# Kernel tuning notes

Measured on AMD Instinct MI355X. Metric: run time of the kernel, lower is better.

Reference implementation:

```python
import jax, jax.numpy as jnp
import numpy as np

ROPE_BASE = 10000.0

def apply_rope(x):
    # x: (BS, T, H, hd). 1D RoPE over temporal axis with rotate-half convention.
    BS, T, H, hd = x.shape
    half = hd // 2
    inv_freq = 1.0 / (ROPE_BASE ** (jnp.arange(0, half, dtype=jnp.float32) / half))
    angles = jnp.arange(T, dtype=jnp.float32)[:, None] * inv_freq[None, :]  # (T, half)
    cos = jnp.concatenate([jnp.cos(angles), jnp.cos(angles)], axis=-1)[None, :, None, :]  # (1,T,1,hd)
    sin = jnp.concatenate([jnp.sin(angles), jnp.sin(angles)], axis=-1)[None, :, None, :]
    x1, x2 = x[..., :half], x[..., half:]
    x_rot = jnp.concatenate([-x2, x1], axis=-1)
    return (x * cos + x_rot * sin).astype(x.dtype)

def setup_inputs() -> dict:
    key = jax.random.key(0)
    ks = jax.random.split(key, 7)
    B, T_p, T_f, S, d = 4, 8, 8, 256, 512
    v_p = jax.random.normal(ks[0], (B, T_p, S, d), dtype=jnp.float32)
    v_f = jax.random.normal(ks[1], (B, T_f, S, d), dtype=jnp.float32)
    a_p = jax.random.normal(ks[2], (B, T_p, d), dtype=jnp.float32)
    a_f = jax.random.normal(ks[3], (B, T_f, d), dtype=jnp.float32)
    W_qkv = jax.random.normal(ks[4], (d, 3 * d), dtype=jnp.float32) * (d ** -0.5)
    W_proj = jax.random.normal(ks[5], (d, d), dtype=jnp.float32) * (d ** -0.5)
    b_proj = jnp.zeros((d,), dtype=jnp.float32)
    return {"v_p": v_p, "v_f": v_f, "a_p": a_p, "a_f": a_f,
            "W_qkv": W_qkv, "W_proj": W_proj, "b_proj": b_proj}

def reference(v_p, v_f, a_p, a_f, W_qkv, W_proj, b_proj):
    num_heads = 8
    B, T_p, S, d = v_p.shape
    T_f = v_f.shape[1]
    hd = d // num_heads
    scale = hd ** -0.5

    # rearrange 'b t s d -> (b s) t d'
    vp = jnp.transpose(v_p, (0, 2, 1, 3)).reshape(B * S, T_p, d)
    vf = jnp.transpose(v_f, (0, 2, 1, 3)).reshape(B * S, T_f, d)
    # repeat 'b t d -> (b s) t d'
    ap = jnp.broadcast_to(a_p[:, None], (B, S, T_p, d)).reshape(B * S, T_p, d)
    af = jnp.broadcast_to(a_f[:, None], (B, S, T_f, d)).reshape(B * S, T_f, d)

    tokens = jnp.concatenate([vp, vf, ap, af], axis=1)  # (BS, total_T, d)
    BS, total_T = tokens.shape[0], tokens.shape[1]

    qkv = tokens @ W_qkv  # (BS, total_T, 3d), no bias
    q, k, v = jnp.split(qkv, 3, axis=-1)
    q = q.reshape(BS, total_T, num_heads, hd)
    k = k.reshape(BS, total_T, num_heads, hd)
    v = v.reshape(BS, total_T, num_heads, hd)

    q = apply_rope(q)
    k = apply_rope(k)

    # joint bidirectional attention over total_T
    attn = jnp.einsum('bthd,bThd->bhtT', q, k) * scale
    attn = jax.nn.softmax(attn, axis=-1)
    out = jnp.einsum('bhtT,bThd->bthd', attn, v).reshape(BS, total_T, d)

    out = out @ W_proj + b_proj

    vp_o = out[:, :T_p]
    vf_o = out[:, T_p:T_p + T_f]
    ap_o = out[:, T_p + T_f:T_p + T_f + T_p]
    af_o = out[:, T_p + T_f + T_p:]

    # '(b s) t d -> b t s d'
    vp_o = jnp.transpose(vp_o.reshape(B, S, T_p, d), (0, 2, 1, 3))
    vf_o = jnp.transpose(vf_o.reshape(B, S, T_f, d), (0, 2, 1, 3))
    # '(b s) t d -> b s t d' then mean over s
    ap_o = ap_o.reshape(B, S, T_p, d).mean(axis=1)
    af_o = af_o.reshape(B, S, T_f, d).mean(axis=1)
    return (vp_o, vf_o, ap_o, af_o)
```

## Files before the change

kernel.cpp:

```cpp
#include <hip/hip_runtime.h>
#include <math.h>

#define BB   4
#define SS   256
#define DD   512
#define HH   8
#define HD   64
#define HALF 32
#define TT   32
#define TV   16
#define W3   1536
#define MROWS  16448
#define MPAD   16512

#define VP_BASE 0
#define VF_BASE 4194304
#define AP_BASE 8388608
#define AF_BASE 8404992

#define LN10000_OVER_HALF (9.210340371976184f / 32.0f)

typedef _Float16 h2 __attribute__((ext_vector_type(2)));
typedef _Float16 h4 __attribute__((ext_vector_type(4)));
typedef _Float16 h8 __attribute__((ext_vector_type(8)));
typedef float    f4 __attribute__((ext_vector_type(4)));
typedef float    f16v __attribute__((ext_vector_type(16)));

__device__ __forceinline__ float ropefreq(int i) {
    return __expf(-(float)i * LN10000_OVER_HALF);
}

typedef __attribute__((address_space(3))) void*       lds_ptr_t;
typedef const __attribute__((address_space(1))) void* gbl_ptr_t;
__device__ __forceinline__ void async16(const void* g, void* l) {
    __builtin_amdgcn_global_load_lds((gbl_ptr_t)g, (lds_ptr_t)l, 16, 0, 0);
}

__global__ __launch_bounds__(256)
void conv_kernel(const float* __restrict__ v_p, const float* __restrict__ v_f,
                 const float* __restrict__ a_p, const float* __restrict__ a_f,
                 const float* __restrict__ Wqkv, const float* __restrict__ Wp,
                 _Float16* __restrict__ tok, _Float16* __restrict__ Wt,
                 _Float16* __restrict__ Wpt) {
    __shared__ float tile[64 * 65];
    const int bid = blockIdx.x, tid = threadIdx.x;
    if (bid < 8224) {
        int id = bid * 256 + tid;
        int e  = id * 4;
        int r  = e >> 9, c = e & 511;
        const float* src;
        if (r < 16384) {
            int bs = r >> 4, t = r & 15, b = bs >> 8, s = bs & 255;
            src = (t < 8) ? v_p + (size_t)((b * 8 + t) * SS + s) * DD
                          : v_f + (size_t)((b * 8 + t - 8) * SS + s) * DD;
        } else {
            int idx = r - 16384, b = idx >> 4, t2 = idx & 15;
            src = (t2 < 8) ? a_p + (size_t)(b * 8 + t2) * DD
                           : a_f + (size_t)(b * 8 + (t2 - 8)) * DD;
        }
        float4 v = *(const float4*)(src + c);
        h4 o = { (_Float16)v.x, (_Float16)v.y, (_Float16)v.z, (_Float16)v.w };
        *(h4*)(tok + (size_t)r * DD + c) = o;
    } else {
        int tb = bid - 8224;
        const float* src; _Float16* dst; int ld, k0, n0;
        if (tb < 192) {
            src = Wqkv; dst = Wt; ld = W3;
            k0 = (tb & 7) * 64; n0 = (tb >> 3) * 64;
        } else {
            int t2 = tb - 192;
            src = Wp; dst = Wpt; ld = DD;
            k0 = (t2 & 7) * 64; n0 = (t2 >> 3) * 64;
        }
#pragma unroll
        for (int p = 0; p < 16; ++p) {
            int idx = p * 256 + tid, rr = idx >> 6, cc = idx & 63;
            tile[rr * 65 + cc] = src[(size_t)(k0 + rr) * ld + n0 + cc];
        }
        __syncthreads();
#pragma unroll
        for (int p = 0; p < 16; ++p) {
            int idx = p * 256 + tid, rr = idx >> 6, cc = idx & 63;
            dst[(size_t)(n0 + rr) * DD + k0 + cc] = (_Float16)tile[cc * 65 + rr];
        }
    }
}

__global__ __launch_bounds__(256, 3)
void gemm_qkv_kernel(const _Float16* __restrict__ A, const _Float16* __restrict__ Bt,
                     _Float16* __restrict__ C) {
    __shared__ __align__(16) _Float16 As[128 * 64];
    __shared__ __align__(16) _Float16 Bs[128 * 64];
    const int tid = threadIdx.x, lane = tid & 63, wave = tid >> 6;
    const int bid = blockIdx.x;
    const int tm = bid / 12, tn = bid % 12;
    const int m_base = (wave >> 1) * 64, n_base = (wave & 1) * 64;
    const int quad = lane >> 4, l16 = lane & 15;

    f4 acc[4][4] = {};

    int srow[4], soff[4];
#pragma unroll
    for (int p = 0; p < 4; ++p) {
        int ci = p * 256 + tid;
        int r = ci >> 3, sl = ci & 7;
        srow[p] = r;
        soff[p] = (sl ^ (r & 7)) * 8;
    }

    for (int k0 = 0; k0 < 512; k0 += 64) {
#pragma unroll
        for (int p = 0; p < 4; ++p) {
            int ci = p * 256 + tid;
            async16(A  + (size_t)(tm * 128 + srow[p]) * 512 + k0 + soff[p],
                    &As[ci * 8]);
            async16(Bt + (size_t)(tn * 128 + srow[p]) * 512 + k0 + soff[p],
                    &Bs[ci * 8]);
        }
        __syncthreads();

#pragma unroll
        for (int kk = 0; kk < 2; ++kk) {
            h8 af[4], bf[4];
#pragma unroll
            for (int mi = 0; mi < 4; ++mi) {
                int m = m_base + mi * 16 + l16;
                int sl = (kk * 4 + quad) ^ (m & 7);
                af[mi] = *(const h8*)&As[m * 64 + sl * 8];
            }
#pragma unroll
            for (int ni = 0; ni < 4; ++ni) {
                int n = n_base + ni * 16 + l16;
                int sl = (kk * 4 + quad) ^ (n & 7);
                bf[ni] = *(const h8*)&Bs[n * 64 + sl * 8];
            }
#pragma unroll
            for (int mi = 0; mi < 4; ++mi)
#pragma unroll
                for (int ni = 0; ni < 4; ++ni)
                    acc[mi][ni] = __builtin_amdgcn_mfma_f32_16x16x32_f16(
                        af[mi], bf[ni], acc[mi][ni], 0, 0, 0);
        }
        __syncthreads();
    }

#pragma unroll
    for (int mi = 0; mi < 4; ++mi)
#pragma unroll
        for (int ni = 0; ni < 4; ++ni) {
            int row = tm * 128 + m_base + mi * 16 + quad * 4;
            int col = tn * 128 + n_base + ni * 16 + l16;
#pragma unroll
            for (int r = 0; r < 4; ++r)
                C[(size_t)(row + r) * W3 + col] = (_Float16)acc[mi][ni][r];
        }
}

__global__ __launch_bounds__(256)
void attn5_kernel(const _Float16* __restrict__ qkv, _Float16* __restrict__ attnv,
                  _Float16* __restrict__ attna) {
    __shared__ _Float16 VlA[4][32 * 72];
    __shared__ _Float16 PlA[4][32 * 40];
    const int bid = blockIdx.x;
    const int bs = bid >> 1, hh = bid & 1, b = bs >> 8, s = bs & 255;
    const int tid = threadIdx.x, wave = tid >> 6, lane = tid & 63;
    const int t = lane & 31, half = lane >> 5;
    _Float16* vl = &VlA[wave][0];
    _Float16* pl = &PlA[wave][0];
    const int h = wave + 4 * hh;

    const size_t row = (t < 16) ? (size_t)(bs * 16 + t)
                                : (size_t)(16384 + b * 16 + (t - 16));
    const _Float16* qp = qkv + row * W3 + h * HD;

    float ccA[8], ssA[8], ccB[8], ssB[8];
#pragma unroll
    for (int j = 0; j < 8; ++j) {
        float aA = (float)t * ropefreq(8 * half + j);
        float aB = (float)t * ropefreq(16 + 8 * half + j);
        __sincosf(aA, &ssA[j], &ccA[j]);
        __sincosf(aB, &ssB[j], &ccB[j]);
    }

    h8 v0 = *(const h8*)(qp + 2 * DD + 32 * half);
    h8 v1 = *(const h8*)(qp + 2 * DD + 32 * half + 8);
    h8 v2 = *(const h8*)(qp + 2 * DD + 32 * half + 16);
    h8 v3 = *(const h8*)(qp + 2 * DD + 32 * half + 24);
    *(h8*)&vl[t * 72 + 32 * half +  0] = v0;
    *(h8*)&vl[t * 72 + 32 * half +  8] = v1;
    *(h8*)&vl[t * 72 + 32 * half + 16] = v2;
    *(h8*)&vl[t * 72 + 32 * half + 24] = v3;

    h8 q0 = *(const h8*)(qp + 8 * half);
    h8 q1 = *(const h8*)(qp + 8 * half + 16);
    h8 q2 = *(const h8*)(qp + 8 * half + 32);
    h8 q3 = *(const h8*)(qp + 8 * half + 48);
    h8 k0 = *(const h8*)(qp + DD + 8 * half);
    h8 k1 = *(const h8*)(qp + DD + 8 * half + 16);
    h8 k2 = *(const h8*)(qp + DD + 8 * half + 32);
    h8 k3 = *(const h8*)(qp + DD + 8 * half + 48);

    h8 qf0, qf1, qf2, qf3, kf0, kf1, kf2, kf3;
#pragma unroll
    for (int j = 0; j < 8; ++j) {
        float x1 = (float)q0[j], x2 = (float)q2[j];
        qf0[j] = (_Float16)(0.125f * (x1 * ccA[j] - x2 * ssA[j]));
        qf2[j] = (_Float16)(0.125f * (x2 * ccA[j] + x1 * ssA[j]));
        x1 = (float)q1[j]; x2 = (float)q3[j];
        qf1[j] = (_Float16)(0.125f * (x1 * ccB[j] - x2 * ssB[j]));
        qf3[j] = (_Float16)(0.125f * (x2 * ccB[j] + x1 * ssB[j]));
        x1 = (float)k0[j]; x2 = (float)k2[j];
        kf0[j] = (_Float16)(x1 * ccA[j] - x2 * ssA[j]);
        kf2[j] = (_Float16)(x2 * ccA[j] + x1 * ssA[j]);
        x1 = (float)k1[j]; x2 = (float)k3[j];
        kf1[j] = (_Float16)(x1 * ccB[j] - x2 * ssB[j]);
        kf3[j] = (_Float16)(x2 * ccB[j] + x1 * ssB[j]);
    }

    f16v s4 = {};
    s4 = __builtin_amdgcn_mfma_f32_32x32x16_f16(qf0, kf0, s4, 0, 0, 0);
    s4 = __builtin_amdgcn_mfma_f32_32x32x16_f16(qf1, kf1, s4, 0, 0, 0);
    s4 = __builtin_amdgcn_mfma_f32_32x32x16_f16(qf2, kf2, s4, 0, 0, 0);
    s4 = __builtin_amdgcn_mfma_f32_32x32x16_f16(qf3, kf3, s4, 0, 0, 0);

#pragma unroll
    for (int r = 0; r < 16; ++r) {
        float m = s4[r];
#pragma unroll
        for (int mask = 1; mask <= 16; mask <<= 1)
            m = fmaxf(m, __shfl_xor(m, mask));
        float e = __expf(s4[r] - m);
        float sm = e;
#pragma unroll
        for (int mask = 1; mask <= 16; mask <<= 1)
            sm += __shfl_xor(sm, mask);
        float p = e / sm;
        int rr = (r & 3) + 8 * (r >> 2) + 4 * half;
        pl[rr * 40 + t] = (_Float16)p;
    }

    f16v o_acc[2];
#pragma unroll
    for (int n0 = 0; n0 < 2; ++n0) {
        f16v o = {};
#pragma unroll
        for (int kk = 0; kk < 2; ++kk) {
            h8 pf = *(const h8*)&pl[t * 40 + kk * 16 + half * 8];
            h8 vf;
#pragma unroll
            for (int jj = 0; jj < 8; ++jj)
                vf[jj] = vl[(kk * 16 + half * 8 + jj) * 72 + n0 * 32 + t];
            o = __builtin_amdgcn_mfma_f32_32x32x16_f16(pf, vf, o, 0, 0, 0);
        }
        o_acc[n0] = o;
    }

#pragma unroll
    for (int n0 = 0; n0 < 2; ++n0)
#pragma unroll
        for (int r = 0; r < 16; ++r) {
            int i = (r & 3) + 8 * (r >> 2) + 4 * half;
            vl[i * 72 + n0 * 32 + t] = (_Float16)o_acc[n0][r];
        }

#pragma unroll
    for (int rr = 0; rr < 4; ++rr) {
        int i = rr * 8 + (lane >> 3);
        int c = (lane & 7) * 8;
        h8 val = *(const h8*)&vl[i * 72 + c];
        if (rr < 2)
            *(h8*)&attnv[(size_t)(bs * 16 + i) * DD + h * HD + c] = val;
        else
            *(h8*)&attna[(((size_t)b * 16 + (i - 16)) * SS + s) * DD + h * HD + c] = val;
    }
}

__global__ __launch_bounds__(256)
void reduce_a_kernel(const _Float16* __restrict__ attna, _Float16* __restrict__ abar) {
    __shared__ float red[4][DD];
    const int r = blockIdx.x;
    const int tid = threadIdx.x;
    const int sg = tid >> 6, cl = tid & 63;

    float acc[8] = {};
    const _Float16* base = attna + ((size_t)r * SS + sg * 64) * DD + cl * 8;
#pragma unroll 4
    for (int i = 0; i < 64; ++i) {
        h8 v = *(const h8*)(base + (size_t)i * DD);
#pragma unroll
        for (int j = 0; j < 8; ++j) acc[j] += (float)v[j];
    }
#pragma unroll
    for (int j = 0; j < 8; ++j) red[sg][cl * 8 + j] = acc[j];
    __syncthreads();

    int c = tid * 2;
    float s0 = red[0][c] + red[1][c] + red[2][c] + red[3][c];
    float s1 = red[0][c + 1] + red[1][c + 1] + red[2][c + 1] + red[3][c + 1];
    h2 o = { (_Float16)(s0 * (1.0f / SS)), (_Float16)(s1 * (1.0f / SS)) };
    *(h2*)&abar[(size_t)r * DD + c] = o;
}

__global__ __launch_bounds__(256, 3)
void proj_kernel(const _Float16* __restrict__ A, const _Float16* __restrict__ Bt,
                 const float* __restrict__ bp, float* __restrict__ out) {
    __shared__ __align__(16) _Float16 As[128 * 64];
    __shared__ __align__(16) _Float16 Bs[128 * 64];
    const int tid = threadIdx.x, lane = tid & 63, wave = tid >> 6;
    const int bid = blockIdx.x;
    const int tm = bid >> 2, tn = bid & 3;
    const int m_base = (wave >> 1) * 64, n_base = (wave & 1) * 64;
    const int quad = lane >> 4, l16 = lane & 15;

    f4 acc[4][4] = {};

    int srow[4], soff[4];
#pragma unroll
    for (int p = 0; p < 4; ++p) {
        int ci = p * 256 + tid;
        int r = ci >> 3, sl = ci & 7;
        srow[p] = r;
        soff[p] = (sl ^ (r & 7)) * 8;
    }

    for (int k0 = 0; k0 < 512; k0 += 64) {
#pragma unroll
        for (int p = 0; p < 4; ++p) {
            int ci = p * 256 + tid;
            async16(A  + (size_t)(tm * 128 + srow[p]) * 512 + k0 + soff[p],
                    &As[ci * 8]);
            async16(Bt + (size_t)(tn * 128 + srow[p]) * 512 + k0 + soff[p],
                    &Bs[ci * 8]);
        }
        __syncthreads();

#pragma unroll
        for (int kk = 0; kk < 2; ++kk) {
            h8 af[4], bf[4];
#pragma unroll
            for (int mi = 0; mi < 4; ++mi) {
                int m = m_base + mi * 16 + l16;
                int sl = (kk * 4 + quad) ^ (m & 7);
                af[mi] = *(const h8*)&As[m * 64 + sl * 8];
            }
#pragma unroll
            for (int ni = 0; ni < 4; ++ni) {
                int n = n_base + ni * 16 + l16;
                int sl = (kk * 4 + quad) ^ (n & 7);
                bf[ni] = *(const h8*)&Bs[n * 64 + sl * 8];
            }
#pragma unroll
            for (int mi = 0; mi < 4; ++mi)
#pragma unroll
                for (int ni = 0; ni < 4; ++ni)
                    acc[mi][ni] = __builtin_amdgcn_mfma_f32_16x16x32_f16(
                        af[mi], bf[ni], acc[mi][ni], 0, 0, 0);
        }
        __syncthreads();
    }

#pragma unroll
    for (int mi = 0; mi < 4; ++mi)
#pragma unroll
        for (int ni = 0; ni < 4; ++ni) {
            int row0 = tm * 128 + m_base + mi * 16 + quad * 4;
            int col  = tn * 128 + n_base + ni * 16 + l16;
            float bias = bp[col];
#pragma unroll
            for (int r = 0; r < 4; ++r) {
                int row = row0 + r;
                float val = acc[mi][ni][r] + bias;
                if (row < 16384) {
                    int bsq = row >> 4, t = row & 15;
                    int b = bsq >> 8, s = bsq & 255;
                    size_t off = (t < 8)
                        ? (VP_BASE + (size_t)((b * 8 + t) * SS + s) * DD + col)
                        : (VF_BASE + (size_t)((b * 8 + t - 8) * SS + s) * DD + col);
                    out[off] = val;
                } else if (row < 16448) {
                    int idx = row - 16384;
                    int b = idx >> 4, t2 = idx & 15;
                    size_t off = (t2 < 8)
                        ? (AP_BASE + (size_t)(b * 8 + t2) * DD + col)
                        : (AF_BASE + (size_t)(b * 8 + (t2 - 8)) * DD + col);
                    out[off] = val;
                }
            }
        }
}

extern "C" void kernel_launch(void* const* d_in, const int* in_sizes, int n_in,
                              void* d_out, int out_size, void* d_ws, size_t ws_size,
                              hipStream_t stream) {
    const float* v_p  = (const float*)d_in[0];
    const float* v_f  = (const float*)d_in[1];
    const float* a_p  = (const float*)d_in[2];
    const float* a_f  = (const float*)d_in[3];
    const float* Wqkv = (const float*)d_in[4];
    const float* Wp   = (const float*)d_in[5];
    const float* bp   = (const float*)d_in[6];
    float* out = (float*)d_out;

    char* w = (char*)d_ws;
    _Float16* tok   = (_Float16*)w;  w += (size_t)MPAD * DD * 2;
    _Float16* qkv   = (_Float16*)w;  w += (size_t)MPAD * W3 * 2;
    _Float16* attnv = (_Float16*)w;  w += (size_t)MPAD * DD * 2;
    _Float16* Wt    = (_Float16*)w;  w += (size_t)W3 * DD * 2;
    _Float16* Wpt   = (_Float16*)w;  w += (size_t)DD * DD * 2;
    _Float16* attna = tok;
    _Float16* abar  = attnv + (size_t)16384 * DD;

    conv_kernel<<<8480, 256, 0, stream>>>(v_p, v_f, a_p, a_f, Wqkv, Wp,
                                          tok, Wt, Wpt);
    gemm_qkv_kernel<<<129 * 12, 256, 0, stream>>>(tok, Wt, qkv);
    attn5_kernel<<<2048, 256, 0, stream>>>(qkv, attnv, attna);
    reduce_a_kernel<<<64, 256, 0, stream>>>(attna, abar);
    proj_kernel<<<129 * 4, 256, 0, stream>>>(attnv, Wpt, bp, out);
}
```

Baseline: 192.8 us.

## Stage GEMM output and attention Q/K loads through LDS for coalesced access

```diff
diff --git a/kernel.cpp b/kernel.cpp
--- a/kernel.cpp
+++ b/kernel.cpp
@@ -89,8 +89,9 @@
 __global__ __launch_bounds__(256, 3)
 void gemm_qkv_kernel(const _Float16* __restrict__ A, const _Float16* __restrict__ Bt,
                      _Float16* __restrict__ C) {
-    __shared__ __align__(16) _Float16 As[128 * 64];
-    __shared__ __align__(16) _Float16 Bs[128 * 64];
+    __shared__ __align__(16) _Float16 smem[128 * 64 * 2];
+    _Float16* As = smem;
+    _Float16* Bs = smem + 128 * 64;
     const int tid = threadIdx.x, lane = tid & 63, wave = tid >> 6;
     const int bid = blockIdx.x;
     const int tm = bid / 12, tn = bid % 12;
@@ -144,34 +145,49 @@
         __syncthreads();
     }
 
+    _Float16* ct = smem + wave * 4096;
 #pragma unroll
     for (int mi = 0; mi < 4; ++mi)
 #pragma unroll
         for (int ni = 0; ni < 4; ++ni) {
-            int row = tm * 128 + m_base + mi * 16 + quad * 4;
-            int col = tn * 128 + n_base + ni * 16 + l16;
+            int lr0 = mi * 16 + quad * 4;
+            int lc  = ni * 16 + l16;
 #pragma unroll
             for (int r = 0; r < 4; ++r)
-                C[(size_t)(row + r) * W3 + col] = (_Float16)acc[mi][ni][r];
-        }
+                ct[(lr0 + r) * 64 + lc] = (_Float16)acc[mi][ni][r];
+        }
+    {
+        const int sr = lane >> 3, c8 = lane & 7;
+#pragma unroll
+        for (int g = 0; g < 8; ++g) {
+            int lr = g * 8 + sr;
+            h8 val = *(const h8*)&ct[lr * 64 + c8 * 8];
+            *(h8*)&C[(size_t)(tm * 128 + m_base + lr) * W3
+                     + tn * 128 + n_base + c8 * 8] = val;
+        }
+    }
 }
 
 __global__ __launch_bounds__(256)
-void attn5_kernel(const _Float16* __restrict__ qkv, _Float16* __restrict__ attnv,
+void attn6_kernel(const _Float16* __restrict__ qkv, _Float16* __restrict__ attnv,
                   _Float16* __restrict__ attna) {
-    __shared__ _Float16 VlA[4][32 * 72];
-    __shared__ _Float16 PlA[4][32 * 40];
-    const int bid = blockIdx.x;
-    const int bs = bid >> 1, hh = bid & 1, b = bs >> 8, s = bs & 255;
+    __shared__ _Float16 T1A[4][32 * 72];
+    __shared__ _Float16 T2A[4][32 * 72];
+    const int bs = blockIdx.x, b = bs >> 8, s = bs & 255;
     const int tid = threadIdx.x, wave = tid >> 6, lane = tid & 63;
     const int t = lane & 31, half = lane >> 5;
-    _Float16* vl = &VlA[wave][0];
-    _Float16* pl = &PlA[wave][0];
-    const int h = wave + 4 * hh;
-
-    const size_t row = (t < 16) ? (size_t)(bs * 16 + t)
-                                : (size_t)(16384 + b * 16 + (t - 16));
-    const _Float16* qp = qkv + row * W3 + h * HD;
+    _Float16* qt = &T1A[wave][0];
+    _Float16* kt = &T2A[wave][0];
+
+    const int sr = lane >> 3, c8 = lane & 7;
+    const _Float16* grp[4];
+#pragma unroll
+    for (int g = 0; g < 4; ++g) {
+        int row = g * 8 + sr;
+        size_t grow = (row < 16) ? (size_t)(bs * 16 + row)
+                                 : (size_t)(16384 + b * 16 + (row - 16));
+        grp[g] = qkv + grow * W3 + c8 * 8;
+    }
 
     float ccA[8], ssA[8], ccB[8], ssB[8];
 #pragma unroll
@@ -182,96 +198,107 @@
         __sincosf(aB, &ssB[j], &ccB[j]);
     }
 
-    h8 v0 = *(const h8*)(qp + 2 * DD + 32 * half);
-    h8 v1 = *(const h8*)(qp + 2 * DD + 32 * half + 8);
-    h8 v2 = *(const h8*)(qp + 2 * DD + 32 * half + 16);
-    h8 v3 = *(const h8*)(qp + 2 * DD + 32 * half + 24);
-    *(h8*)&vl[t * 72 + 32 * half +  0] = v0;
-    *(h8*)&vl[t * 72 + 32 * half +  8] = v1;
-    *(h8*)&vl[t * 72 + 32 * half + 16] = v2;
-    *(h8*)&vl[t * 72 + 32 * half + 24] = v3;
-
-    h8 q0 = *(const h8*)(qp + 8 * half);
-    h8 q1 = *(const h8*)(qp + 8 * half + 16);
-    h8 q2 = *(const h8*)(qp + 8 * half + 32);
-    h8 q3 = *(const h8*)(qp + 8 * half + 48);
-    h8 k0 = *(const h8*)(qp + DD + 8 * half);
-    h8 k1 = *(const h8*)(qp + DD + 8 * half + 16);
-    h8 k2 = *(const h8*)(qp + DD + 8 * half + 32);
-    h8 k3 = *(const h8*)(qp + DD + 8 * half + 48);
-
-    h8 qf0, qf1, qf2, qf3, kf0, kf1, kf2, kf3;
-#pragma unroll
-    for (int j = 0; j < 8; ++j) {
-        float x1 = (float)q0[j], x2 = (float)q2[j];
-        qf0[j] = (_Float16)(0.125f * (x1 * ccA[j] - x2 * ssA[j]));
-        qf2[j] = (_Float16)(0.125f * (x2 * ccA[j] + x1 * ssA[j]));
-        x1 = (float)q1[j]; x2 = (float)q3[j];
-        qf1[j] = (_Float16)(0.125f * (x1 * ccB[j] - x2 * ssB[j]));
-        qf3[j] = (_Float16)(0.125f * (x2 * ccB[j] + x1 * ssB[j]));
-        x1 = (float)k0[j]; x2 = (float)k2[j];
-        kf0[j] = (_Float16)(x1 * ccA[j] - x2 * ssA[j]);
-        kf2[j] = (_Float16)(x2 * ccA[j] + x1 * ssA[j]);
-        x1 = (float)k1[j]; x2 = (float)k3[j];
-        kf1[j] = (_Float16)(x1 * ccB[j] - x2 * ssB[j]);
-        kf3[j] = (_Float16)(x2 * ccB[j] + x1 * ssB[j]);
-    }
-
-    f16v s4 = {};
-    s4 = __builtin_amdgcn_mfma_f32_32x32x16_f16(qf0, kf0, s4, 0, 0, 0);
-    s4 = __builtin_amdgcn_mfma_f32_32x32x16_f16(qf1, kf1, s4, 0, 0, 0);
-    s4 = __builtin_amdgcn_mfma_f32_32x32x16_f16(qf2, kf2, s4, 0, 0, 0);
-    s4 = __builtin_amdgcn_mfma_f32_32x32x16_f16(qf3, kf3, s4, 0, 0, 0);
-
-#pragma unroll
-    for (int r = 0; r < 16; ++r) {
-        float m = s4[r];
-#pragma unroll
-        for (int mask = 1; mask <= 16; mask <<= 1)
-            m = fmaxf(m, __shfl_xor(m, mask));
-        float e = __expf(s4[r] - m);
-        float sm = e;
-#pragma unroll
-        for (int mask = 1; mask <= 16; mask <<= 1)
-            sm += __shfl_xor(sm, mask);
-        float p = e / sm;
-        int rr = (r & 3) + 8 * (r >> 2) + 4 * half;
-        pl[rr * 40 + t] = (_Float16)p;
-    }
-
-    f16v o_acc[2];
-#pragma unroll
-    for (int n0 = 0; n0 < 2; ++n0) {
-        f16v o = {};
-#pragma unroll
-        for (int kk = 0; kk < 2; ++kk) {
-            h8 pf = *(const h8*)&pl[t * 40 + kk * 16 + half * 8];
-            h8 vf;
-#pragma unroll
-            for (int jj = 0; jj < 8; ++jj)
-                vf[jj] = vl[(kk * 16 + half * 8 + jj) * 72 + n0 * 32 + t];
-            o = __builtin_amdgcn_mfma_f32_32x32x16_f16(pf, vf, o, 0, 0, 0);
-        }
-        o_acc[n0] = o;
-    }
-
-#pragma unroll
-    for (int n0 = 0; n0 < 2; ++n0)
+    for (int hh = 0; hh < 2; ++hh) {
+        const int h = wave + 4 * hh;
+        const int cb = h * HD;
+
+#pragma unroll
+        for (int g = 0; g < 4; ++g) {
+            int row = g * 8 + sr;
+            h8 qv = *(const h8*)(grp[g] + cb);
+            h8 kv = *(const h8*)(grp[g] + DD + cb);
+            *(h8*)&qt[row * 72 + c8 * 8] = qv;
+            *(h8*)&kt[row * 72 + c8 * 8] = kv;
+        }
+
+        h8 q0 = *(const h8*)&qt[t * 72 + 8 * half];
+        h8 q1 = *(const h8*)&qt[t * 72 + 16 + 8 * half];
+        h8 q2 = *(const h8*)&qt[t * 72 + 32 + 8 * half];
+        h8 q3 = *(const h8*)&qt[t * 72 + 48 + 8 * half];
+        h8 k0 = *(const h8*)&kt[t * 72 + 8 * half];
+        h8 k1 = *(const h8*)&kt[t * 72 + 16 + 8 * half];
+        h8 k2 = *(const h8*)&kt[t * 72 + 32 + 8 * half];
+        h8 k3 = *(const h8*)&kt[t * 72 + 48 + 8 * half];
+
+#pragma unroll
+        for (int g = 0; g < 4; ++g) {
+            int row = g * 8 + sr;
+            h8 vv = *(const h8*)(grp[g] + 2 * DD + cb);
+            *(h8*)&qt[row * 72 + c8 * 8] = vv;
+        }
+
+        h8 qf0, qf1, qf2, qf3, kf0, kf1, kf2, kf3;
+#pragma unroll
+        for (int j = 0; j < 8; ++j) {
+            float x1 = (float)q0[j], x2 = (float)q2[j];
+            qf0[j] = (_Float16)(0.125f * (x1 * ccA[j] - x2 * ssA[j]));
+            qf2[j] = (_Float16)(0.125f * (x2 * ccA[j] + x1 * ssA[j]));
+            x1 = (float)q1[j]; x2 = (float)q3[j];
+            qf1[j] = (_Float16)(0.125f * (x1 * ccB[j] - x2 * ssB[j]));
+            qf3[j] = (_Float16)(0.125f * (x2 * ccB[j] + x1 * ssB[j]));
+            x1 = (float)k0[j]; x2 = (float)k2[j];
+            kf0[j] = (_Float16)(x1 * ccA[j] - x2 * ssA[j]);
+            kf2[j] = (_Float16)(x2 * ccA[j] + x1 * ssA[j]);
+            x1 = (float)k1[j]; x2 = (float)k3[j];
+            kf1[j] = (_Float16)(x1 * ccB[j] - x2 * ssB[j]);
+            kf3[j] = (_Float16)(x2 * ccB[j] + x1 * ssB[j]);
+        }
+
+        f16v s4 = {};
+        s4 = __builtin_amdgcn_mfma_f32_32x32x16_f16(qf0, kf0, s4, 0, 0, 0);
+        s4 = __builtin_amdgcn_mfma_f32_32x32x16_f16(qf1, kf1, s4, 0, 0, 0);
+        s4 = __builtin_amdgcn_mfma_f32_32x32x16_f16(qf2, kf2, s4, 0, 0, 0);
+        s4 = __builtin_amdgcn_mfma_f32_32x32x16_f16(qf3, kf3, s4, 0, 0, 0);
+
 #pragma unroll
         for (int r = 0; r < 16; ++r) {
-            int i = (r & 3) + 8 * (r >> 2) + 4 * half;
-            vl[i * 72 + n0 * 32 + t] = (_Float16)o_acc[n0][r];
-        }
-
-#pragma unroll
-    for (int rr = 0; rr < 4; ++rr) {
-        int i = rr * 8 + (lane >> 3);
-        int c = (lane & 7) * 8;
-        h8 val = *(const h8*)&vl[i * 72 + c];
-        if (rr < 2)
-            *(h8*)&attnv[(size_t)(bs * 16 + i) * DD + h * HD + c] = val;
-        else
-            *(h8*)&attna[(((size_t)b * 16 + (i - 16)) * SS + s) * DD + h * HD + c] = val;
+            float m = s4[r];
+#pragma unroll
+            for (int mask = 1; mask <= 16; mask <<= 1)
+                m = fmaxf(m, __shfl_xor(m, mask));
+            float e = __expf(s4[r] - m);
+            float sm = e;
+#pragma unroll
+            for (int mask = 1; mask <= 16; mask <<= 1)
+                sm += __shfl_xor(sm, mask);
+            float p = e / sm;
+            int rr = (r & 3) + 8 * (r >> 2) + 4 * half;
+            kt[rr * 72 + t] = (_Float16)p;
+        }
+
+        f16v o_acc[2];
+#pragma unroll
+        for (int n0 = 0; n0 < 2; ++n0) {
+            f16v o = {};
+#pragma unroll
+            for (int kk = 0; kk < 2; ++kk) {
+                h8 pf = *(const h8*)&kt[t * 72 + kk * 16 + half * 8];
+                h8 vf;
+#pragma unroll
+                for (int jj = 0; jj < 8; ++jj)
+                    vf[jj] = qt[(kk * 16 + half * 8 + jj) * 72 + n0 * 32 + t];
+                o = __builtin_amdgcn_mfma_f32_32x32x16_f16(pf, vf, o, 0, 0, 0);
+            }
+            o_acc[n0] = o;
+        }
+
+#pragma unroll
+        for (int n0 = 0; n0 < 2; ++n0)
+#pragma unroll
+            for (int r = 0; r < 16; ++r) {
+                int i = (r & 3) + 8 * (r >> 2) + 4 * half;
+                kt[i * 72 + n0 * 32 + t] = (_Float16)o_acc[n0][r];
+            }
+#pragma unroll
+        for (int rr = 0; rr < 4; ++rr) {
+            int i = rr * 8 + sr;
+            int c = c8 * 8;
+            h8 val = *(const h8*)&kt[i * 72 + c];
+            if (rr < 2)
+                *(h8*)&attnv[(size_t)(bs * 16 + i) * DD + h * HD + c] = val;
+            else
+                *(h8*)&attna[(((size_t)b * 16 + (i - 16)) * SS + s) * DD + h * HD + c] = val;
+        }
     }
 }
 
@@ -413,7 +440,7 @@
     conv_kernel<<<8480, 256, 0, stream>>>(v_p, v_f, a_p, a_f, Wqkv, Wp,
                                           tok, Wt, Wpt);
     gemm_qkv_kernel<<<129 * 12, 256, 0, stream>>>(tok, Wt, qkv);
-    attn5_kernel<<<2048, 256, 0, stream>>>(qkv, attnv, attna);
+    attn6_kernel<<<1024, 256, 0, stream>>>(qkv, attnv, attna);
     reduce_a_kernel<<<64, 256, 0, stream>>>(attna, abar);
     proj_kernel<<<129 * 4, 256, 0, stream>>>(attnv, Wpt, bp, out);
 }
```

After: 197.1 us. 1.02x slower.
